# Performance work log

Measured on AMD Instinct MI355X. Metric: run time of the kernel, lower is better.

## Reference

```python
import jax, jax.numpy as jnp
import numpy as np

N, C, K = 262144, 64, 27  # active voxels, channels, 3^3 kernel offsets


def setup_inputs() -> dict:
    key = jax.random.key(0)
    k1, k2, k3, k4, k5, k6, k7 = jax.random.split(key, 7)
    features = jax.random.normal(k1, (N, C), dtype=jnp.float32)
    # kernel map: for each offset k and output voxel n, index of contributing input voxel
    nbr_idx = jax.random.randint(k2, (K, N), 0, N, dtype=jnp.int32)
    mask = jax.random.uniform(k3, (K, N)) < 0.4
    scale = 1.0 / np.sqrt(K * C)
    w1 = jax.random.normal(k4, (K, C, C), dtype=jnp.float32) * scale
    b1 = jax.random.normal(k5, (C,), dtype=jnp.float32) * 0.01
    w2 = jax.random.normal(k6, (K, C, C), dtype=jnp.float32) * scale
    b2 = jax.random.normal(k7, (C,), dtype=jnp.float32) * 0.01
    return dict(features=features, nbr_idx=nbr_idx, mask=mask,
                w1=w1, b1=b1, w2=w2, b2=b2)


def _sparse_conv(feat, nbr_idx, mask, W, b):
    """Explicit-GEMM sparse conv: per kernel offset, gather -> GEMM -> accumulate."""
    def step(acc, xs):
        idx, m, Wk = xs                                  # [N], [N], [C, C]
        g = feat[idx] * m[:, None].astype(feat.dtype)    # gather + zero invalid: [N, C]
        return acc + g @ Wk, None
    acc, _ = jax.lax.scan(step, jnp.zeros_like(feat), (nbr_idx, mask, W))
    return acc + b


def reference(features, nbr_idx, mask, w1, b1, w2, b2):
    h = _sparse_conv(features, nbr_idx, mask, w1, b1)
    h = _sparse_conv(h, nbr_idx, mask, w2, b2)
    return h + features  # residual add of input feature tensor
```

## Files before the change

### kernel.cpp

```cpp
#include <hip/hip_runtime.h>
#include <stdint.h>

#define N_VOX 262144
#define CCH 64
#define KOFF 27

typedef short v8s __attribute__((ext_vector_type(8)));
typedef float v4f __attribute__((ext_vector_type(4)));
typedef int   v4i __attribute__((ext_vector_type(4)));

__device__ __forceinline__ unsigned short f2bf(float f) {
  unsigned u = __float_as_uint(f);
  u += 0x7fff + ((u >> 16) & 1);
  return (unsigned short)(u >> 16);
}

__global__ void prep_flag_k(const unsigned* __restrict__ m, int* __restrict__ flag) {
  if (threadIdx.x == 0) {
    int wordlike = 1;
    for (int i = 0; i < 256; ++i) {
      unsigned v = m[i];
      if (v > 1u && v != 0x3f800000u) { wordlike = 0; break; }
    }
    *flag = wordlike ? 0 : 2;
  }
}

__global__ void prep_mask_k(const void* __restrict__ m, const int* __restrict__ flag,
                            unsigned char* __restrict__ mb, int n) {
  int f = *flag;
  for (int i = blockIdx.x * blockDim.x + threadIdx.x; i < n; i += gridDim.x * blockDim.x) {
    unsigned char v;
    if (f == 2) v = (((const unsigned char*)m)[i] != 0);
    else        v = (((const unsigned*)m)[i] != 0u);
    mb[i] = v;
  }
}

__global__ void prep_feat_k(const float* __restrict__ src, unsigned short* __restrict__ dst, int n8) {
  int i = blockIdx.x * blockDim.x + threadIdx.x;
  if (i >= n8) return;
  const float4* s4 = (const float4*)src;
  float4 a = s4[i * 2], b = s4[i * 2 + 1];
  v8s v;
  v[0] = (short)f2bf(a.x); v[1] = (short)f2bf(a.y);
  v[2] = (short)f2bf(a.z); v[3] = (short)f2bf(a.w);
  v[4] = (short)f2bf(b.x); v[5] = (short)f2bf(b.y);
  v[6] = (short)f2bf(b.z); v[7] = (short)f2bf(b.w);
  ((v8s*)dst)[i] = v;
}

__global__ void prep_w_k(const float* __restrict__ w, unsigned short* __restrict__ wt) {
  int i = blockIdx.x * blockDim.x + threadIdx.x;
  if (i >= KOFF * CCH * CCH) return;
  int k = i >> 12, rem = i & 4095, kk = rem >> 6, col = rem & 63;
  wt[(k << 12) + (col << 6) + (kk ^ ((col & 7) << 3))] = f2bf(w[i]);
}

template <int LAYER>
__global__ __launch_bounds__(256, 4)
void conv_layer_k(const v8s* __restrict__ src, const int* __restrict__ nbr,
                  const unsigned char* __restrict__ mb,
                  const v4i* __restrict__ wt, const float* __restrict__ bias,
                  const float* __restrict__ resid, void* __restrict__ outp) {
  __shared__ v4i ldsB[2][512];
  const int tid = threadIdx.x;
  const int lane = tid & 63;
  const int wv = tid >> 6;
  const int l15 = lane & 15;
  const int g = lane >> 4;
  const int rowbase = blockIdx.x * 128 + wv * 32;
  const int r0 = rowbase + l15;
  const int r1 = rowbase + 16 + l15;

  ldsB[0][tid] = wt[tid];
  ldsB[0][256 + tid] = wt[256 + tid];

  v8s a0c = {}, a1c = {}, a2c = {}, a3c = {};
  {
    int i0 = nbr[r0], i1 = nbr[r1];
    if (mb[r0]) { a0c = src[i0 * 8 + g]; a1c = src[i0 * 8 + 4 + g]; }
    if (mb[r1]) { a2c = src[i1 * 8 + g]; a3c = src[i1 * 8 + 4 + g]; }
  }
  int j0 = nbr[N_VOX + r0], j1 = nbr[N_VOX + r1];
  bool n0 = mb[N_VOX + r0], n1 = mb[N_VOX + r1];

  v4f acc0[4] = {}, acc1[4] = {};
  __syncthreads();

  int cur = 0;
  for (int k = 0; k < KOFF; ++k) {
    const int kc1 = (k + 1 < KOFF) ? k + 1 : KOFF - 1;
    const int kc2 = (k + 2 < KOFF) ? k + 2 : KOFF - 1;

    v4i nw0 = wt[kc1 * 512 + tid];
    v4i nw1 = wt[kc1 * 512 + 256 + tid];

    int t0 = nbr[kc2 * N_VOX + r0], t1 = nbr[kc2 * N_VOX + r1];
    bool u0 = mb[kc2 * N_VOX + r0], u1 = mb[kc2 * N_VOX + r1];

    v8s a0n = {}, a1n = {}, a2n = {}, a3n = {};
    if (k + 1 < KOFF) {
      if (n0) { a0n = src[j0 * 8 + g]; a1n = src[j0 * 8 + 4 + g]; }
      if (n1) { a2n = src[j1 * 8 + g]; a3n = src[j1 * 8 + 4 + g]; }
    }

    const short* Bs = (const short*)ldsB[cur];
    v8s bf0[4], bf1[4];
#pragma unroll
    for (int ct = 0; ct < 4; ++ct) {
      int col = ct * 16 + l15;
      int sw = (col & 7) << 3;
      int base = col << 6;
      bf0[ct] = *(const v8s*)(Bs + base + ((g * 8) ^ sw));
      bf1[ct] = *(const v8s*)(Bs + base + ((32 + g * 8) ^ sw));
    }

#pragma unroll
    for (int ct = 0; ct < 4; ++ct) {
      acc0[ct] = __builtin_amdgcn_mfma_f32_16x16x32_bf16(a0c, bf0[ct], acc0[ct], 0, 0, 0);
      acc0[ct] = __builtin_amdgcn_mfma_f32_16x16x32_bf16(a1c, bf1[ct], acc0[ct], 0, 0, 0);
      acc1[ct] = __builtin_amdgcn_mfma_f32_16x16x32_bf16(a2c, bf0[ct], acc1[ct], 0, 0, 0);
      acc1[ct] = __builtin_amdgcn_mfma_f32_16x16x32_bf16(a3c, bf1[ct], acc1[ct], 0, 0, 0);
    }

    ldsB[cur ^ 1][tid] = nw0;
    ldsB[cur ^ 1][256 + tid] = nw1;
    __syncthreads();
    cur ^= 1;

    a0c = a0n; a1c = a1n; a2c = a2n; a3c = a3n;
    j0 = t0; j1 = t1; n0 = u0; n1 = u1;
  }

  float bv[4];
#pragma unroll
  for (int ct = 0; ct < 4; ++ct) bv[ct] = bias[ct * 16 + l15];

#pragma unroll
  for (int rt = 0; rt < 2; ++rt) {
    int row0 = rowbase + rt * 16 + g * 4;
#pragma unroll
    for (int ct = 0; ct < 4; ++ct) {
      int col = ct * 16 + l15;
      const v4f& a = rt ? acc1[ct] : acc0[ct];
#pragma unroll
      for (int i = 0; i < 4; ++i) {
        float v = a[i] + bv[ct];
        int o = (row0 + i) * CCH + col;
        if (LAYER == 1) ((unsigned short*)outp)[o] = f2bf(v);
        else            ((float*)outp)[o] = v + resid[o];
      }
    }
  }
}

extern "C" void kernel_launch(void* const* d_in, const int* in_sizes, int n_in,
                              void* d_out, int out_size, void* d_ws, size_t ws_size,
                              hipStream_t stream) {
  const float* feat = (const float*)d_in[0];
  const int* nbr    = (const int*)d_in[1];
  const void* mask  = d_in[2];
  const float* w1   = (const float*)d_in[3];
  const float* b1   = (const float*)d_in[4];
  const float* w2   = (const float*)d_in[5];
  const float* b2   = (const float*)d_in[6];

  char* ws = (char*)d_ws;
  unsigned short* featb = (unsigned short*)ws;
  unsigned short* hb    = (unsigned short*)(ws + 33554432);
  unsigned char*  maskb = (unsigned char*)(ws + 67108864);
  unsigned short* wt1   = (unsigned short*)(ws + 74186752);
  unsigned short* wt2   = (unsigned short*)(ws + 74407936);
  int*            flag  = (int*)(ws + 74629120);

  prep_flag_k<<<1, 64, 0, stream>>>((const unsigned*)mask, flag);
  prep_mask_k<<<4096, 256, 0, stream>>>(mask, flag, maskb, KOFF * N_VOX);
  prep_feat_k<<<8192, 256, 0, stream>>>(feat, featb, N_VOX * CCH / 8);
  prep_w_k<<<432, 256, 0, stream>>>(w1, wt1);
  prep_w_k<<<432, 256, 0, stream>>>(w2, wt2);

  conv_layer_k<1><<<2048, 256, 0, stream>>>((const v8s*)featb, nbr, maskb,
                                            (const v4i*)wt1, b1, nullptr, (void*)hb);
  conv_layer_k<2><<<2048, 256, 0, stream>>>((const v8s*)hb, nbr, maskb,
                                            (const v4i*)wt2, b2, feat, (void*)d_out);
}
```

Measured before the change: 216.5 us.

## Deepen gather prefetch pipeline and use barrier that keeps vector loads in flight

Raises the software pipeline depth for neighbor feature gathers: feature rows are now fetched two offsets ahead and index/mask loads four offsets ahead, using more registers to hold in-flight data. Replaces __syncthreads with a custom barrier that waits only on LDS counters, so outstanding global gathers are not drained at each iteration's barrier. Launch bounds occupancy hint drops from 4 to 3 blocks to make room for the extra registers, trading occupancy for memory-level parallelism within each wave.

```diff
diff --git a/kernel.cpp b/kernel.cpp
--- a/kernel.cpp
+++ b/kernel.cpp
@@ -57,8 +57,14 @@
   wt[(k << 12) + (col << 6) + (kk ^ ((col & 7) << 3))] = f2bf(w[i]);
 }
 
+__device__ __forceinline__ void barrier_keep_vmem() {
+  asm volatile("s_waitcnt lgkmcnt(0)" ::: "memory");
+  __builtin_amdgcn_s_barrier();
+  __builtin_amdgcn_sched_barrier(0);
+}
+
 template <int LAYER>
-__global__ __launch_bounds__(256, 4)
+__global__ __launch_bounds__(256, 3)
 void conv_layer_k(const v8s* __restrict__ src, const int* __restrict__ nbr,
                   const unsigned char* __restrict__ mb,
                   const v4i* __restrict__ wt, const float* __restrict__ bias,
@@ -73,37 +79,44 @@
   const int r0 = rowbase + l15;
   const int r1 = rowbase + 16 + l15;
 
-  ldsB[0][tid] = wt[tid];
-  ldsB[0][256 + tid] = wt[256 + tid];
+  v4i w0a = wt[tid], w0b = wt[256 + tid];
+
+  int i0_0 = nbr[r0],             i0_1 = nbr[r1];
+  int i1_0 = nbr[N_VOX + r0],     i1_1 = nbr[N_VOX + r1];
+  int i2_0 = nbr[2 * N_VOX + r0], i2_1 = nbr[2 * N_VOX + r1];
+  int i3_0 = nbr[3 * N_VOX + r0], i3_1 = nbr[3 * N_VOX + r1];
+  bool m0_0 = mb[r0],             m0_1 = mb[r1];
+  bool m1_0 = mb[N_VOX + r0],     m1_1 = mb[N_VOX + r1];
+  bool m2_0 = mb[2 * N_VOX + r0], m2_1 = mb[2 * N_VOX + r1];
+  bool m3_0 = mb[3 * N_VOX + r0], m3_1 = mb[3 * N_VOX + r1];
 
   v8s a0c = {}, a1c = {}, a2c = {}, a3c = {};
-  {
-    int i0 = nbr[r0], i1 = nbr[r1];
-    if (mb[r0]) { a0c = src[i0 * 8 + g]; a1c = src[i0 * 8 + 4 + g]; }
-    if (mb[r1]) { a2c = src[i1 * 8 + g]; a3c = src[i1 * 8 + 4 + g]; }
-  }
-  int j0 = nbr[N_VOX + r0], j1 = nbr[N_VOX + r1];
-  bool n0 = mb[N_VOX + r0], n1 = mb[N_VOX + r1];
+  if (m0_0) { a0c = src[i0_0 * 8 + g]; a1c = src[i0_0 * 8 + 4 + g]; }
+  if (m0_1) { a2c = src[i0_1 * 8 + g]; a3c = src[i0_1 * 8 + 4 + g]; }
+  v8s a0n = {}, a1n = {}, a2n = {}, a3n = {};
+  if (m1_0) { a0n = src[i1_0 * 8 + g]; a1n = src[i1_0 * 8 + 4 + g]; }
+  if (m1_1) { a2n = src[i1_1 * 8 + g]; a3n = src[i1_1 * 8 + 4 + g]; }
+
+  ldsB[0][tid] = w0a;
+  ldsB[0][256 + tid] = w0b;
+  barrier_keep_vmem();
 
   v4f acc0[4] = {}, acc1[4] = {};
-  __syncthreads();
-
   int cur = 0;
+
   for (int k = 0; k < KOFF; ++k) {
     const int kc1 = (k + 1 < KOFF) ? k + 1 : KOFF - 1;
-    const int kc2 = (k + 2 < KOFF) ? k + 2 : KOFF - 1;
+    const int kc4 = (k + 4 < KOFF) ? k + 4 : KOFF - 1;
+
+    v8s a0f = {}, a1f = {}, a2f = {}, a3f = {};
+    if (m2_0) { a0f = src[i2_0 * 8 + g]; a1f = src[i2_0 * 8 + 4 + g]; }
+    if (m2_1) { a2f = src[i2_1 * 8 + g]; a3f = src[i2_1 * 8 + 4 + g]; }
 
     v4i nw0 = wt[kc1 * 512 + tid];
     v4i nw1 = wt[kc1 * 512 + 256 + tid];
 
-    int t0 = nbr[kc2 * N_VOX + r0], t1 = nbr[kc2 * N_VOX + r1];
-    bool u0 = mb[kc2 * N_VOX + r0], u1 = mb[kc2 * N_VOX + r1];
-
-    v8s a0n = {}, a1n = {}, a2n = {}, a3n = {};
-    if (k + 1 < KOFF) {
-      if (n0) { a0n = src[j0 * 8 + g]; a1n = src[j0 * 8 + 4 + g]; }
-      if (n1) { a2n = src[j1 * 8 + g]; a3n = src[j1 * 8 + 4 + g]; }
-    }
+    int t0 = nbr[kc4 * N_VOX + r0], t1 = nbr[kc4 * N_VOX + r1];
+    bool u0 = mb[kc4 * N_VOX + r0], u1 = mb[kc4 * N_VOX + r1];
 
     const short* Bs = (const short*)ldsB[cur];
     v8s bf0[4], bf1[4];
@@ -126,11 +139,13 @@
 
     ldsB[cur ^ 1][tid] = nw0;
     ldsB[cur ^ 1][256 + tid] = nw1;
-    __syncthreads();
+    barrier_keep_vmem();
     cur ^= 1;
 
     a0c = a0n; a1c = a1n; a2c = a2n; a3c = a3n;
-    j0 = t0; j1 = t1; n0 = u0; n1 = u1;
+    a0n = a0f; a1n = a1f; a2n = a2f; a3n = a3f;
+    i2_0 = i3_0; i2_1 = i3_1; m2_0 = m3_0; m2_1 = m3_1;
+    i3_0 = t0;   i3_1 = t1;   m3_0 = u0;   m3_1 = u1;
   }
 
   float bv[4];
```

Result: slower. 234.9 us (+8.5%).

## Drop LDS weight staging and deepen gather prefetch with even/odd register pipelines

Applied to the files above, without the earlier changes.

Each wave now loads its weight B-fragments straight from global memory (L2/L1-resident, unswizzled layout) into registers instead of double-buffering them through LDS. That removes the per-offset __syncthreads and the LDS traffic. The gathered feature rows now go through two alternating register sets (even and odd offsets), so gathers are issued about two offsets ahead and neighbor indices about four ahead. This hides more gather latency but raises register pressure under launch_bounds(256,4), and every wave fetches the weights redundantly from cache.

```diff
diff --git a/kernel.cpp b/kernel.cpp
--- a/kernel.cpp
+++ b/kernel.cpp
@@ -7,7 +7,6 @@
 
 typedef short v8s __attribute__((ext_vector_type(8)));
 typedef float v4f __attribute__((ext_vector_type(4)));
-typedef int   v4i __attribute__((ext_vector_type(4)));
 
 __device__ __forceinline__ unsigned short f2bf(float f) {
   unsigned u = __float_as_uint(f);
@@ -54,16 +53,52 @@
   int i = blockIdx.x * blockDim.x + threadIdx.x;
   if (i >= KOFF * CCH * CCH) return;
   int k = i >> 12, rem = i & 4095, kk = rem >> 6, col = rem & 63;
-  wt[(k << 12) + (col << 6) + (kk ^ ((col & 7) << 3))] = f2bf(w[i]);
+  wt[(k << 12) + (col << 6) + kk] = f2bf(w[i]);
+}
+
+__device__ __forceinline__ void conv_body(
+    int k, bool last,
+    const v8s* __restrict__ src, const int* __restrict__ nbr,
+    const unsigned char* __restrict__ mb, const v8s* __restrict__ wptr,
+    int r0, int r1, int g, int l15,
+    v8s& a0, v8s& a1, v8s& a2, v8s& a3,
+    v8s (&bu)[8], int& j0, int& j1, bool& n0, bool& n1,
+    v4f (&acc0)[4], v4f (&acc1)[4])
+{
+#pragma unroll
+  for (int ct = 0; ct < 4; ++ct) {
+    acc0[ct] = __builtin_amdgcn_mfma_f32_16x16x32_bf16(a0, bu[ct],     acc0[ct], 0, 0, 0);
+    acc0[ct] = __builtin_amdgcn_mfma_f32_16x16x32_bf16(a1, bu[4 + ct], acc0[ct], 0, 0, 0);
+    acc1[ct] = __builtin_amdgcn_mfma_f32_16x16x32_bf16(a2, bu[ct],     acc1[ct], 0, 0, 0);
+    acc1[ct] = __builtin_amdgcn_mfma_f32_16x16x32_bf16(a3, bu[4 + ct], acc1[ct], 0, 0, 0);
+  }
+  if (last) return;
+
+  const int wk = (k + 1) << 9;
+#pragma unroll
+  for (int ct = 0; ct < 4; ++ct) {
+    const int wb = ((ct * 16 + l15) << 3) + g;
+    bu[ct]     = wptr[wk + wb];
+    bu[4 + ct] = wptr[wk + wb + 4];
+  }
+
+  if (k + 2 < KOFF) {
+    a0 = {}; a1 = {}; a2 = {}; a3 = {};
+    if (n0) { a0 = src[j0 * 8 + g]; a1 = src[j0 * 8 + 4 + g]; }
+    if (n1) { a2 = src[j1 * 8 + g]; a3 = src[j1 * 8 + 4 + g]; }
+  }
+
+  const int kj = (k + 4 < KOFF) ? k + 4 : KOFF - 1;
+  j0 = nbr[kj * N_VOX + r0]; j1 = nbr[kj * N_VOX + r1];
+  n0 = mb[kj * N_VOX + r0];  n1 = mb[kj * N_VOX + r1];
 }
 
 template <int LAYER>
 __global__ __launch_bounds__(256, 4)
 void conv_layer_k(const v8s* __restrict__ src, const int* __restrict__ nbr,
                   const unsigned char* __restrict__ mb,
-                  const v4i* __restrict__ wt, const float* __restrict__ bias,
+                  const v8s* __restrict__ wptr, const float* __restrict__ bias,
                   const float* __restrict__ resid, void* __restrict__ outp) {
-  __shared__ v4i ldsB[2][512];
   const int tid = threadIdx.x;
   const int lane = tid & 63;
   const int wv = tid >> 6;
@@ -73,65 +108,41 @@
   const int r0 = rowbase + l15;
   const int r1 = rowbase + 16 + l15;
 
-  ldsB[0][tid] = wt[tid];
-  ldsB[0][256 + tid] = wt[256 + tid];
+  int jE0 = nbr[r0], jE1 = nbr[r1];
+  int jO0 = nbr[N_VOX + r0], jO1 = nbr[N_VOX + r1];
+  bool nE0 = mb[r0], nE1 = mb[r1];
+  bool nO0 = mb[N_VOX + r0], nO1 = mb[N_VOX + r1];
 
-  v8s a0c = {}, a1c = {}, a2c = {}, a3c = {};
-  {
-    int i0 = nbr[r0], i1 = nbr[r1];
-    if (mb[r0]) { a0c = src[i0 * 8 + g]; a1c = src[i0 * 8 + 4 + g]; }
-    if (mb[r1]) { a2c = src[i1 * 8 + g]; a3c = src[i1 * 8 + 4 + g]; }
+  v8s aE0 = {}, aE1 = {}, aE2 = {}, aE3 = {};
+  v8s aO0 = {}, aO1 = {}, aO2 = {}, aO3 = {};
+  if (nE0) { aE0 = src[jE0 * 8 + g]; aE1 = src[jE0 * 8 + 4 + g]; }
+  if (nE1) { aE2 = src[jE1 * 8 + g]; aE3 = src[jE1 * 8 + 4 + g]; }
+  if (nO0) { aO0 = src[jO0 * 8 + g]; aO1 = src[jO0 * 8 + 4 + g]; }
+  if (nO1) { aO2 = src[jO1 * 8 + g]; aO3 = src[jO1 * 8 + 4 + g]; }
+
+  jE0 = nbr[2 * N_VOX + r0]; jE1 = nbr[2 * N_VOX + r1];
+  nE0 = mb[2 * N_VOX + r0];  nE1 = mb[2 * N_VOX + r1];
+  jO0 = nbr[3 * N_VOX + r0]; jO1 = nbr[3 * N_VOX + r1];
+  nO0 = mb[3 * N_VOX + r0];  nO1 = mb[3 * N_VOX + r1];
+
+  v8s bu[8];
+#pragma unroll
+  for (int ct = 0; ct < 4; ++ct) {
+    const int wb = ((ct * 16 + l15) << 3) + g;
+    bu[ct]     = wptr[wb];
+    bu[4 + ct] = wptr[wb + 4];
   }
-  int j0 = nbr[N_VOX + r0], j1 = nbr[N_VOX + r1];
-  bool n0 = mb[N_VOX + r0], n1 = mb[N_VOX + r1];
 
   v4f acc0[4] = {}, acc1[4] = {};
-  __syncthreads();
 
-  int cur = 0;
-  for (int k = 0; k < KOFF; ++k) {
-    const int kc1 = (k + 1 < KOFF) ? k + 1 : KOFF - 1;
-    const int kc2 = (k + 2 < KOFF) ? k + 2 : KOFF - 1;
-
-    v4i nw0 = wt[kc1 * 512 + tid];
-    v4i nw1 = wt[kc1 * 512 + 256 + tid];
-
-    int t0 = nbr[kc2 * N_VOX + r0], t1 = nbr[kc2 * N_VOX + r1];
-    bool u0 = mb[kc2 * N_VOX + r0], u1 = mb[kc2 * N_VOX + r1];
-
-    v8s a0n = {}, a1n = {}, a2n = {}, a3n = {};
-    if (k + 1 < KOFF) {
-      if (n0) { a0n = src[j0 * 8 + g]; a1n = src[j0 * 8 + 4 + g]; }
-      if (n1) { a2n = src[j1 * 8 + g]; a3n = src[j1 * 8 + 4 + g]; }
-    }
-
-    const short* Bs = (const short*)ldsB[cur];
-    v8s bf0[4], bf1[4];
-#pragma unroll
-    for (int ct = 0; ct < 4; ++ct) {
-      int col = ct * 16 + l15;
-      int sw = (col & 7) << 3;
-      int base = col << 6;
-      bf0[ct] = *(const v8s*)(Bs + base + ((g * 8) ^ sw));
-      bf1[ct] = *(const v8s*)(Bs + base + ((32 + g * 8) ^ sw));
-    }
-
-#pragma unroll
-    for (int ct = 0; ct < 4; ++ct) {
-      acc0[ct] = __builtin_amdgcn_mfma_f32_16x16x32_bf16(a0c, bf0[ct], acc0[ct], 0, 0, 0);
-      acc0[ct] = __builtin_amdgcn_mfma_f32_16x16x32_bf16(a1c, bf1[ct], acc0[ct], 0, 0, 0);
-      acc1[ct] = __builtin_amdgcn_mfma_f32_16x16x32_bf16(a2c, bf0[ct], acc1[ct], 0, 0, 0);
-      acc1[ct] = __builtin_amdgcn_mfma_f32_16x16x32_bf16(a3c, bf1[ct], acc1[ct], 0, 0, 0);
-    }
-
-    ldsB[cur ^ 1][tid] = nw0;
-    ldsB[cur ^ 1][256 + tid] = nw1;
-    __syncthreads();
-    cur ^= 1;
-
-    a0c = a0n; a1c = a1n; a2c = a2n; a3c = a3n;
-    j0 = t0; j1 = t1; n0 = u0; n1 = u1;
+  for (int k = 0; k < KOFF - 1; k += 2) {
+    conv_body(k,     false, src, nbr, mb, wptr, r0, r1, g, l15,
+              aE0, aE1, aE2, aE3, bu, jE0, jE1, nE0, nE1, acc0, acc1);
+    conv_body(k + 1, false, src, nbr, mb, wptr, r0, r1, g, l15,
+              aO0, aO1, aO2, aO3, bu, jO0, jO1, nO0, nO1, acc0, acc1);
   }
+  conv_body(KOFF - 1, true, src, nbr, mb, wptr, r0, r1, g, l15,
+            aE0, aE1, aE2, aE3, bu, jE0, jE1, nE0, nE1, acc0, acc1);
 
   float bv[4];
 #pragma unroll
@@ -181,7 +192,7 @@
   prep_w_k<<<432, 256, 0, stream>>>(w2, wt2);
 
   conv_layer_k<1><<<2048, 256, 0, stream>>>((const v8s*)featb, nbr, maskb,
-                                            (const v4i*)wt1, b1, nullptr, (void*)hb);
+                                            (const v8s*)wt1, b1, nullptr, (void*)hb);
   conv_layer_k<2><<<2048, 256, 0, stream>>>((const v8s*)hb, nbr, maskb,
-                                            (const v4i*)wt2, b2, feat, (void*)d_out);
+                                            (const v8s*)wt2, b2, feat, (void*)d_out);
 }
```

Result: slower. 561.3 us (+159.3%).
